# Optimization experiments

Hardware: AMD Instinct MI355X
Metric: run time of the kernel (lower is better)

## Reference

```python
import jax, jax.numpy as jnp
import numpy as np

L = 8        # number of node layers in the DAG
D = 64       # width of every node layer
B = 262144   # batch
N_CONN = L * (L - 1) // 2  # 28 all-to-all forward connections


def setup_inputs() -> dict:
    key = jax.random.key(0)
    kx, kw, kb = jax.random.split(key, 3)
    x = jax.random.normal(kx, (B, D), dtype=jnp.float32)
    # connection weights, torch Linear convention: y = x @ W.T + b, W is [out, in]
    Ws = jax.random.normal(kw, (N_CONN, D, D), dtype=jnp.float32) * (1.0 / np.sqrt(D))
    bs = jax.random.normal(kb, (N_CONN, D), dtype=jnp.float32) * 0.1
    return {"x": x, "Ws": Ws, "bs": bs}


def reference(x, Ws, bs):
    # outputs[0] = input; outputs[1..L-1] start at zero and accumulate messages.
    outs = [x] + [jnp.zeros((x.shape[0], D), dtype=x.dtype) for _ in range(L - 1)]
    # Same iteration order as the torch double loop: source i ascending,
    # target offset i2 ascending; connection c maps layer i -> layer i+i2+1.
    c = 0
    for i in range(L):
        for i2 in range(L - 1 - i):
            j = i + i2 + 1
            outs[j] = outs[j] + jax.nn.relu(outs[i] @ Ws[c].T + bs[c])
            c += 1
    return outs[L - 1]
```

## Files before the change

kernel.cpp:

```cpp
#include <hip/hip_runtime.h>


#define DD 64
#define NCONN 28
#define THREADS 256
#define ROWS_PER_BLOCK 64
#define MAT_ELEMS 4096

typedef __bf16 bf16x8 __attribute__((ext_vector_type(8)));
typedef float f32x4 __attribute__((ext_vector_type(4)));
typedef unsigned short u16x8 __attribute__((ext_vector_type(8)));

__device__ constexpr int OFFS[7] = {0, 7, 13, 18, 22, 25, 27};
__device__ constexpr int CONN[28] = {0, 1,7, 2,8,13, 3,9,14,18, 4,10,15,19,22,
                                     5,11,16,20,23,25, 6,12,17,21,24,26,27};

__device__ __forceinline__ unsigned short f2bfu(float f) {
    return __builtin_bit_cast(unsigned short, (__bf16)f);
}

__device__ __forceinline__ f32x4 vmax4(f32x4 a, f32x4 b) {
#if __has_builtin(__builtin_elementwise_max)
    return __builtin_elementwise_max(a, b);
#else
    f32x4 r;
    r[0] = fmaxf(a[0], b[0]); r[1] = fmaxf(a[1], b[1]);
    r[2] = fmaxf(a[2], b[2]); r[3] = fmaxf(a[3], b[3]);
    return r;
#endif
}

__device__ __forceinline__ void gll16(const unsigned short* g, unsigned short* l) {
    __builtin_amdgcn_global_load_lds(
        (const __attribute__((address_space(1))) unsigned int*)g,
        (__attribute__((address_space(3))) unsigned int*)l, 16, 0, 0);
}

__device__ __forceinline__ void lds_barrier() {
    asm volatile("s_waitcnt lgkmcnt(0)" ::: "memory");
    __builtin_amdgcn_s_barrier();
    asm volatile("" ::: "memory");
}

__global__ void wconv_kernel(const float* __restrict__ w,
                             unsigned short* __restrict__ o) {
    int i = blockIdx.x * blockDim.x + threadIdx.x;
    if (i >= NCONN * 512) return;
    int conn = i >> 9;
    int within = i & 511;
    int r  = within >> 3;
    int k0 = (within & 7) << 3;
    const float* src = w + conn * MAT_ELEMS + r * DD + k0;
    float4 v0 = *reinterpret_cast<const float4*>(src);
    float4 v1 = *reinterpret_cast<const float4*>(src + 4);
    u16x8 d;
    d[0] = f2bfu(v0.x); d[1] = f2bfu(v0.y); d[2] = f2bfu(v0.z); d[3] = f2bfu(v0.w);
    d[4] = f2bfu(v1.x); d[5] = f2bfu(v1.y); d[6] = f2bfu(v1.z); d[7] = f2bfu(v1.w);
    *reinterpret_cast<u16x8*>(o + conn * MAT_ELEMS + r * DD + (k0 ^ ((r & 7) << 3))) = d;
}

template <bool GLL>
__global__ __launch_bounds__(THREADS, 3)
void dag_kernel(const float* __restrict__ x,
                const float* __restrict__ Wf,
                const unsigned short* __restrict__ Wimg,
                const float* __restrict__ bs,
                float* __restrict__ out) {
    __shared__ __align__(16) unsigned short ring[4 * MAT_ELEMS];
    __shared__ __align__(16) unsigned short sB[2 * 2048];
    __shared__ __align__(16) float sBias[NCONN * DD];

    const int tid  = threadIdx.x;
    const int lane = tid & 63;
    const int wv   = tid >> 6;
    const int pair = wv >> 1;
    const int h    = wv & 1;
    const int l15  = lane & 15;
    const int kg   = lane >> 4;

    const long rowbase = (long)blockIdx.x * ROWS_PER_BLOCK + pair * 32;

    for (int idx = tid; idx < NCONN * DD / 4; idx += THREADS)
        reinterpret_cast<float4*>(sBias)[idx] = reinterpret_cast<const float4*>(bs)[idx];

    bf16x8 afrag[7][2][2];
#pragma unroll
    for (int rt = 0; rt < 2; ++rt) {
        const float* xr = x + (rowbase + rt * 16 + l15) * DD;
#pragma unroll
        for (int s = 0; s < 2; ++s) {
            float4 v0 = *reinterpret_cast<const float4*>(xr + s * 32 + kg * 8);
            float4 v1 = *reinterpret_cast<const float4*>(xr + s * 32 + kg * 8 + 4);
            bf16x8 f;
            f[0] = (__bf16)v0.x; f[1] = (__bf16)v0.y; f[2] = (__bf16)v0.z; f[3] = (__bf16)v0.w;
            f[4] = (__bf16)v1.x; f[5] = (__bf16)v1.y; f[6] = (__bf16)v1.z; f[7] = (__bf16)v1.w;
            afrag[0][rt][s] = f;
        }
    }

    auto stage_gll = [&](int p) {
        const unsigned short* src = Wimg + CONN[p] * MAT_ELEMS + wv * 512 + lane * 8;
        unsigned short* dst = ring + (p & 3) * MAT_ELEMS + wv * 512;
#pragma unroll
        for (int hh = 0; hh < 2; ++hh)
            gll16(src + hh * 2048, dst + hh * 2048);
    };
    auto stage_direct = [&](int p) {
        const float* wp = Wf + CONN[p] * MAT_ELEMS;
#pragma unroll
        for (int hh = 0; hh < 2; ++hh) {
            const int e0 = hh * 2048 + tid * 8;
            float4 a0 = *reinterpret_cast<const float4*>(wp + e0);
            float4 a1 = *reinterpret_cast<const float4*>(wp + e0 + 4);
            u16x8 d;
            d[0] = f2bfu(a0.x); d[1] = f2bfu(a0.y); d[2] = f2bfu(a0.z); d[3] = f2bfu(a0.w);
            d[4] = f2bfu(a1.x); d[5] = f2bfu(a1.y); d[6] = f2bfu(a1.z); d[7] = f2bfu(a1.w);
            const int r = e0 >> 6, k0 = e0 & 63;
            *reinterpret_cast<u16x8*>(ring + (p & 3) * MAT_ELEMS +
                                      r * DD + (k0 ^ ((r & 7) << 3))) = d;
        }
    };

    if constexpr (GLL) { stage_gll(0); stage_gll(1); }
    __syncthreads();

    unsigned short* myPB = sB + pair * 2048;
    f32x4 acc[2][2];

#pragma unroll
    for (int j = 1; j <= 7; ++j) {
#pragma unroll
        for (int rt = 0; rt < 2; ++rt)
#pragma unroll
            for (int t = 0; t < 2; ++t) {
                acc[rt][t][0] = 0.f; acc[rt][t][1] = 0.f;
                acc[rt][t][2] = 0.f; acc[rt][t][3] = 0.f;
            }

#pragma unroll
        for (int i = 0; i < j; ++i) {
            const int p = j * (j - 1) / 2 + i;
            const int c = OFFS[i] + (j - i - 1);

            if constexpr (GLL) {
                if ((p & 1) == 0) {
                    if (p > 0) __syncthreads();
                    if (p + 2 < NCONN) { stage_gll(p + 2); stage_gll(p + 3); }
                }
            } else {
                __syncthreads();
                stage_direct(p);
                __syncthreads();
            }

            const unsigned short* wsl = ring + (p & 3) * MAT_ELEMS;
            __builtin_amdgcn_s_setprio(1);
#pragma unroll
            for (int t = 0; t < 2; ++t) {
                const int n  = h * 32 + t * 16 + l15;
                const int xo = (n & 7) << 3;
                u16x8 rw0 = *reinterpret_cast<const u16x8*>(wsl + n * DD + ((kg * 8) ^ xo));
                u16x8 rw1 = *reinterpret_cast<const u16x8*>(wsl + n * DD + ((32 + kg * 8) ^ xo));
                const float bv = sBias[c * DD + n];
                const f32x4 b4 = {bv, bv, bv, bv};
#pragma unroll
                for (int rt = 0; rt < 2; ++rt) {
                    f32x4 C = acc[rt][t];
                    C = __builtin_amdgcn_mfma_f32_16x16x32_bf16(
                            afrag[i][rt][0], __builtin_bit_cast(bf16x8, rw0), C, 0, 0, 0);
                    C = __builtin_amdgcn_mfma_f32_16x16x32_bf16(
                            afrag[i][rt][1], __builtin_bit_cast(bf16x8, rw1), C, 0, 0, 0);
                    acc[rt][t] = vmax4(C + b4, acc[rt][t]);
                }
            }
            __builtin_amdgcn_s_setprio(0);
        }

        if (j < 7) {
#pragma unroll
            for (int rt = 0; rt < 2; ++rt)
#pragma unroll
                for (int t = 0; t < 2; ++t) {
                    const int f = h * 32 + t * 16 + l15;
#pragma unroll
                    for (int q = 0; q < 4; ++q) {
                        const int mr = rt * 16 + kg * 4 + q;
                        myPB[mr * DD + (f ^ ((mr & 7) << 3))] = f2bfu(acc[rt][t][q]);
                    }
                }
            lds_barrier();
#pragma unroll
            for (int rt = 0; rt < 2; ++rt)
#pragma unroll
                for (int s = 0; s < 2; ++s) {
                    u16x8 ra = *reinterpret_cast<const u16x8*>(
                        &myPB[(rt * 16 + l15) * DD + ((s * 32 + kg * 8) ^ ((l15 & 7) << 3))]);
                    afrag[j][rt][s] = __builtin_bit_cast(bf16x8, ra);
                }
            lds_barrier();
        } else {
            float* orow = out + rowbase * DD;
#pragma unroll
            for (int rt = 0; rt < 2; ++rt)
#pragma unroll
                for (int t = 0; t < 2; ++t)
#pragma unroll
                    for (int q = 0; q < 4; ++q)
                        orow[(rt * 16 + kg * 4 + q) * DD + h * 32 + t * 16 + l15] =
                            acc[rt][t][q];
        }
    }
}

extern "C" void kernel_launch(void* const* d_in, const int* in_sizes, int n_in,
                              void* d_out, int out_size, void* d_ws, size_t ws_size,
                              hipStream_t stream) {
    const float* x  = (const float*)d_in[0];
    const float* Ws = (const float*)d_in[1];
    const float* bs = (const float*)d_in[2];
    float* out = (float*)d_out;

    const int nrows = in_sizes[0] / DD;
    const int grid  = nrows / ROWS_PER_BLOCK;

    const size_t wbf_bytes = (size_t)NCONN * MAT_ELEMS * sizeof(unsigned short);
    if (ws_size >= wbf_bytes) {
        unsigned short* wbf = (unsigned short*)d_ws;
        wconv_kernel<<<(NCONN * 512 + 255) / 256, 256, 0, stream>>>(Ws, wbf);
        dag_kernel<true><<<grid, THREADS, 0, stream>>>(x, Ws, wbf, bs, out);
    } else {
        dag_kernel<false><<<grid, THREADS, 0, stream>>>(x, Ws, nullptr, bs, out);
    }
}
```

Baseline: 102.4 us.

## Shrink block to 32 rows with four waves each owning a 16-column slice

Halves rows per block to 32 so all four waves share one 32-row tile, each computing a 16-output-column slice instead of two wave pairs splitting 64 rows. This doubles grid size and halves per-wave accumulators and register pressure, which may raise occupancy, but weight staging from global/L2 is amortized over half as many rows. Bias is now folded into the MFMA accumulator input rather than added afterwards.

Result: slower. 150.8 us (+47.3%).

```diff
diff --git a/kernel.cpp b/kernel.cpp
--- a/kernel.cpp
+++ b/kernel.cpp
@@ -4,7 +4,7 @@
 #define DD 64
 #define NCONN 28
 #define THREADS 256
-#define ROWS_PER_BLOCK 64
+#define ROWS_PER_BLOCK 32
 #define MAT_ELEMS 4096
 
 typedef __bf16 bf16x8 __attribute__((ext_vector_type(8)));
@@ -67,18 +67,16 @@
                 const float* __restrict__ bs,
                 float* __restrict__ out) {
     __shared__ __align__(16) unsigned short ring[4 * MAT_ELEMS];
-    __shared__ __align__(16) unsigned short sB[2 * 2048];
+    __shared__ __align__(16) unsigned short sB[2048];
     __shared__ __align__(16) float sBias[NCONN * DD];
 
     const int tid  = threadIdx.x;
     const int lane = tid & 63;
     const int wv   = tid >> 6;
-    const int pair = wv >> 1;
-    const int h    = wv & 1;
     const int l15  = lane & 15;
     const int kg   = lane >> 4;
 
-    const long rowbase = (long)blockIdx.x * ROWS_PER_BLOCK + pair * 32;
+    const long rowbase = (long)blockIdx.x * ROWS_PER_BLOCK;
 
     for (int idx = tid; idx < NCONN * DD / 4; idx += THREADS)
         reinterpret_cast<float4*>(sBias)[idx] = reinterpret_cast<const float4*>(bs)[idx];
@@ -99,11 +97,11 @@
     }
 
     auto stage_gll = [&](int p) {
-        const unsigned short* src = Wimg + CONN[p] * MAT_ELEMS + wv * 512 + lane * 8;
-        unsigned short* dst = ring + (p & 3) * MAT_ELEMS + wv * 512;
+        const unsigned short* src = Wimg + CONN[p] * MAT_ELEMS + wv * 1024 + lane * 8;
+        unsigned short* dst = ring + (p & 3) * MAT_ELEMS + wv * 1024;
 #pragma unroll
         for (int hh = 0; hh < 2; ++hh)
-            gll16(src + hh * 2048, dst + hh * 2048);
+            gll16(src + hh * 512, dst + hh * 512);
     };
     auto stage_direct = [&](int p) {
         const float* wp = Wf + CONN[p] * MAT_ELEMS;
@@ -124,18 +122,14 @@
     if constexpr (GLL) { stage_gll(0); stage_gll(1); }
     __syncthreads();
 
-    unsigned short* myPB = sB + pair * 2048;
-    f32x4 acc[2][2];
+    f32x4 acc[2];
 
 #pragma unroll
     for (int j = 1; j <= 7; ++j) {
 #pragma unroll
-        for (int rt = 0; rt < 2; ++rt)
-#pragma unroll
-            for (int t = 0; t < 2; ++t) {
-                acc[rt][t][0] = 0.f; acc[rt][t][1] = 0.f;
-                acc[rt][t][2] = 0.f; acc[rt][t][3] = 0.f;
-            }
+        for (int rt = 0; rt < 2; ++rt) {
+            acc[rt][0] = 0.f; acc[rt][1] = 0.f; acc[rt][2] = 0.f; acc[rt][3] = 0.f;
+        }
 
 #pragma unroll
         for (int i = 0; i < j; ++i) {
@@ -154,47 +148,43 @@
             }
 
             const unsigned short* wsl = ring + (p & 3) * MAT_ELEMS;
+            const int n  = wv * 16 + l15;
+            const int xo = (n & 7) << 3;
+            u16x8 rw0 = *reinterpret_cast<const u16x8*>(wsl + n * DD + ((kg * 8) ^ xo));
+            u16x8 rw1 = *reinterpret_cast<const u16x8*>(wsl + n * DD + ((32 + kg * 8) ^ xo));
+            const float bv = sBias[c * DD + n];
+            const f32x4 b4 = {bv, bv, bv, bv};
+
             __builtin_amdgcn_s_setprio(1);
 #pragma unroll
-            for (int t = 0; t < 2; ++t) {
-                const int n  = h * 32 + t * 16 + l15;
-                const int xo = (n & 7) << 3;
-                u16x8 rw0 = *reinterpret_cast<const u16x8*>(wsl + n * DD + ((kg * 8) ^ xo));
-                u16x8 rw1 = *reinterpret_cast<const u16x8*>(wsl + n * DD + ((32 + kg * 8) ^ xo));
-                const float bv = sBias[c * DD + n];
-                const f32x4 b4 = {bv, bv, bv, bv};
-#pragma unroll
-                for (int rt = 0; rt < 2; ++rt) {
-                    f32x4 C = acc[rt][t];
-                    C = __builtin_amdgcn_mfma_f32_16x16x32_bf16(
-                            afrag[i][rt][0], __builtin_bit_cast(bf16x8, rw0), C, 0, 0, 0);
-                    C = __builtin_amdgcn_mfma_f32_16x16x32_bf16(
-                            afrag[i][rt][1], __builtin_bit_cast(bf16x8, rw1), C, 0, 0, 0);
-                    acc[rt][t] = vmax4(C + b4, acc[rt][t]);
+            for (int rt = 0; rt < 2; ++rt) {
+                f32x4 C = acc[rt] + b4;
+                C = __builtin_amdgcn_mfma_f32_16x16x32_bf16(
+                        afrag[i][rt][0], __builtin_bit_cast(bf16x8, rw0), C, 0, 0, 0);
+                C = __builtin_amdgcn_mfma_f32_16x16x32_bf16(
+                        afrag[i][rt][1], __builtin_bit_cast(bf16x8, rw1), C, 0, 0, 0);
+                acc[rt] = vmax4(C, acc[rt]);
+            }
+            __builtin_amdgcn_s_setprio(0);
+        }
+
+        if (j < 7) {
+#pragma unroll
+            for (int rt = 0; rt < 2; ++rt) {
+                const int f = wv * 16 + l15;
+#pragma unroll
+                for (int q = 0; q < 4; ++q) {
+                    const int mr = rt * 16 + kg * 4 + q;
+                    sB[mr * DD + (f ^ ((mr & 7) << 3))] = f2bfu(acc[rt][q]);
                 }
             }
-            __builtin_amdgcn_s_setprio(0);
-        }
-
-        if (j < 7) {
-#pragma unroll
-            for (int rt = 0; rt < 2; ++rt)
-#pragma unroll
-                for (int t = 0; t < 2; ++t) {
-                    const int f = h * 32 + t * 16 + l15;
-#pragma unroll
-                    for (int q = 0; q < 4; ++q) {
-                        const int mr = rt * 16 + kg * 4 + q;
-                        myPB[mr * DD + (f ^ ((mr & 7) << 3))] = f2bfu(acc[rt][t][q]);
-                    }
-                }
             lds_barrier();
 #pragma unroll
             for (int rt = 0; rt < 2; ++rt)
 #pragma unroll
                 for (int s = 0; s < 2; ++s) {
                     u16x8 ra = *reinterpret_cast<const u16x8*>(
-                        &myPB[(rt * 16 + l15) * DD + ((s * 32 + kg * 8) ^ ((l15 & 7) << 3))]);
+                        &sB[(rt * 16 + l15) * DD + ((s * 32 + kg * 8) ^ ((l15 & 7) << 3))]);
                     afrag[j][rt][s] = __builtin_bit_cast(bf16x8, ra);
                 }
             lds_barrier();
@@ -203,11 +193,8 @@
 #pragma unroll
             for (int rt = 0; rt < 2; ++rt)
 #pragma unroll
-                for (int t = 0; t < 2; ++t)
-#pragma unroll
-                    for (int q = 0; q < 4; ++q)
-                        orow[(rt * 16 + kg * 4 + q) * DD + h * 32 + t * 16 + l15] =
-                            acc[rt][t][q];
+                for (int q = 0; q < 4; ++q)
+                    orow[(rt * 16 + kg * 4 + q) * DD + wv * 16 + l15] = acc[rt][q];
         }
     }
 }
```

## Halve rows per block, prefetch bias into registers, fold bias into MFMA accumulator

Applied to the files above, without the earlier changes.

Each block now handles 32 rows instead of 64, so each wave pair computes one 16-row tile rather than two. This cuts the afrag/acc register footprint, and the occupancy hint rises from 3 to 4. The shared-memory bias table is replaced by per-connection bias values loaded into registers alongside the weight prefetch. The bias is now added to the accumulator input before the MFMA instead of after it. The trade-off is that each staged weight matrix is reused across half as many rows, which doubles weight LDS traffic and global weight loads per output row.

After: 130.5 us. 27.5% more time.

```diff
diff --git a/kernel.cpp b/kernel.cpp
--- a/kernel.cpp
+++ b/kernel.cpp
@@ -4,7 +4,7 @@
 #define DD 64
 #define NCONN 28
 #define THREADS 256
-#define ROWS_PER_BLOCK 64
+#define ROWS_PER_BLOCK 32
 #define MAT_ELEMS 4096
 
 typedef __bf16 bf16x8 __attribute__((ext_vector_type(8)));
@@ -60,15 +60,14 @@
 }
 
 template <bool GLL>
-__global__ __launch_bounds__(THREADS, 3)
+__global__ __launch_bounds__(THREADS, 4)
 void dag_kernel(const float* __restrict__ x,
                 const float* __restrict__ Wf,
                 const unsigned short* __restrict__ Wimg,
                 const float* __restrict__ bs,
                 float* __restrict__ out) {
     __shared__ __align__(16) unsigned short ring[4 * MAT_ELEMS];
-    __shared__ __align__(16) unsigned short sB[2 * 2048];
-    __shared__ __align__(16) float sBias[NCONN * DD];
+    __shared__ __align__(16) unsigned short sB[2 * 1024];
 
     const int tid  = threadIdx.x;
     const int lane = tid & 63;
@@ -78,15 +77,11 @@
     const int l15  = lane & 15;
     const int kg   = lane >> 4;
 
-    const long rowbase = (long)blockIdx.x * ROWS_PER_BLOCK + pair * 32;
-
-    for (int idx = tid; idx < NCONN * DD / 4; idx += THREADS)
-        reinterpret_cast<float4*>(sBias)[idx] = reinterpret_cast<const float4*>(bs)[idx];
-
-    bf16x8 afrag[7][2][2];
-#pragma unroll
-    for (int rt = 0; rt < 2; ++rt) {
-        const float* xr = x + (rowbase + rt * 16 + l15) * DD;
+    const long rowbase = (long)blockIdx.x * ROWS_PER_BLOCK + pair * 16;
+
+    bf16x8 afrag[7][2];
+    {
+        const float* xr = x + (rowbase + l15) * DD;
 #pragma unroll
         for (int s = 0; s < 2; ++s) {
             float4 v0 = *reinterpret_cast<const float4*>(xr + s * 32 + kg * 8);
@@ -94,9 +89,16 @@
             bf16x8 f;
             f[0] = (__bf16)v0.x; f[1] = (__bf16)v0.y; f[2] = (__bf16)v0.z; f[3] = (__bf16)v0.w;
             f[4] = (__bf16)v1.x; f[5] = (__bf16)v1.y; f[6] = (__bf16)v1.z; f[7] = (__bf16)v1.w;
-            afrag[0][rt][s] = f;
+            afrag[0][s] = f;
         }
     }
+
+    float breg[2][2][2];
+    auto loadBias = [&](int p) {
+        const float* bp = bs + CONN[p] * DD + h * 32 + l15;
+        float* b = breg[(p >> 1) & 1][p & 1];
+        b[0] = bp[0]; b[1] = bp[16];
+    };
 
     auto stage_gll = [&](int p) {
         const unsigned short* src = Wimg + CONN[p] * MAT_ELEMS + wv * 512 + lane * 8;
@@ -121,39 +123,39 @@
         }
     };
 
+    loadBias(0); loadBias(1);
     if constexpr (GLL) { stage_gll(0); stage_gll(1); }
     __syncthreads();
 
-    unsigned short* myPB = sB + pair * 2048;
-    f32x4 acc[2][2];
+    unsigned short* myPB = sB + pair * 1024;
+    f32x4 acc[2];
 
 #pragma unroll
     for (int j = 1; j <= 7; ++j) {
 #pragma unroll
-        for (int rt = 0; rt < 2; ++rt)
-#pragma unroll
-            for (int t = 0; t < 2; ++t) {
-                acc[rt][t][0] = 0.f; acc[rt][t][1] = 0.f;
-                acc[rt][t][2] = 0.f; acc[rt][t][3] = 0.f;
-            }
+        for (int t = 0; t < 2; ++t) {
+            acc[t][0] = 0.f; acc[t][1] = 0.f; acc[t][2] = 0.f; acc[t][3] = 0.f;
+        }
 
 #pragma unroll
         for (int i = 0; i < j; ++i) {
             const int p = j * (j - 1) / 2 + i;
-            const int c = OFFS[i] + (j - i - 1);
 
             if constexpr (GLL) {
                 if ((p & 1) == 0) {
                     if (p > 0) __syncthreads();
+                    if (p + 2 < NCONN) { loadBias(p + 2); loadBias(p + 3); }
                     if (p + 2 < NCONN) { stage_gll(p + 2); stage_gll(p + 3); }
                 }
             } else {
                 __syncthreads();
                 stage_direct(p);
+                loadBias(p);
                 __syncthreads();
             }
 
             const unsigned short* wsl = ring + (p & 3) * MAT_ELEMS;
+            const float* bv = breg[(p >> 1) & 1][p & 1];
             __builtin_amdgcn_s_setprio(1);
 #pragma unroll
             for (int t = 0; t < 2; ++t) {
@@ -161,53 +163,42 @@
                 const int xo = (n & 7) << 3;
                 u16x8 rw0 = *reinterpret_cast<const u16x8*>(wsl + n * DD + ((kg * 8) ^ xo));
                 u16x8 rw1 = *reinterpret_cast<const u16x8*>(wsl + n * DD + ((32 + kg * 8) ^ xo));
-                const float bv = sBias[c * DD + n];
-                const f32x4 b4 = {bv, bv, bv, bv};
-#pragma unroll
-                for (int rt = 0; rt < 2; ++rt) {
-                    f32x4 C = acc[rt][t];
-                    C = __builtin_amdgcn_mfma_f32_16x16x32_bf16(
-                            afrag[i][rt][0], __builtin_bit_cast(bf16x8, rw0), C, 0, 0, 0);
-                    C = __builtin_amdgcn_mfma_f32_16x16x32_bf16(
-                            afrag[i][rt][1], __builtin_bit_cast(bf16x8, rw1), C, 0, 0, 0);
-                    acc[rt][t] = vmax4(C + b4, acc[rt][t]);
+                const f32x4 b4 = {bv[t], bv[t], bv[t], bv[t]};
+                f32x4 C = acc[t] + b4;
+                C = __builtin_amdgcn_mfma_f32_16x16x32_bf16(
+                        afrag[i][0], __builtin_bit_cast(bf16x8, rw0), C, 0, 0, 0);
+                C = __builtin_amdgcn_mfma_f32_16x16x32_bf16(
+                        afrag[i][1], __builtin_bit_cast(bf16x8, rw1), C, 0, 0, 0);
+                acc[t] = vmax4(C, acc[t]);
+            }
+            __builtin_amdgcn_s_setprio(0);
+        }
+
+        if (j < 7) {
+#pragma unroll
+            for (int t = 0; t < 2; ++t) {
+                const int f = h * 32 + t * 16 + l15;
+#pragma unroll
+                for (int q = 0; q < 4; ++q) {
+                    const int mr = kg * 4 + q;
+                    myPB[mr * DD + (f ^ ((mr & 7) << 3))] = f2bfu(acc[t][q]);
                 }
             }
-            __builtin_amdgcn_s_setprio(0);
-        }
-
-        if (j < 7) {
-#pragma unroll
-            for (int rt = 0; rt < 2; ++rt)
-#pragma unroll
-                for (int t = 0; t < 2; ++t) {
-                    const int f = h * 32 + t * 16 + l15;
-#pragma unroll
-                    for (int q = 0; q < 4; ++q) {
-                        const int mr = rt * 16 + kg * 4 + q;
-                        myPB[mr * DD + (f ^ ((mr & 7) << 3))] = f2bfu(acc[rt][t][q]);
-                    }
-                }
             lds_barrier();
 #pragma unroll
-            for (int rt = 0; rt < 2; ++rt)
-#pragma unroll
-                for (int s = 0; s < 2; ++s) {
-                    u16x8 ra = *reinterpret_cast<const u16x8*>(
-                        &myPB[(rt * 16 + l15) * DD + ((s * 32 + kg * 8) ^ ((l15 & 7) << 3))]);
-                    afrag[j][rt][s] = __builtin_bit_cast(bf16x8, ra);
-                }
+            for (int s = 0; s < 2; ++s) {
+                u16x8 ra = *reinterpret_cast<const u16x8*>(
+                    &myPB[l15 * DD + ((s * 32 + kg * 8) ^ ((l15 & 7) << 3))]);
+                afrag[j][s] = __builtin_bit_cast(bf16x8, ra);
+            }
             lds_barrier();
         } else {
             float* orow = out + rowbase * DD;
 #pragma unroll
-            for (int rt = 0; rt < 2; ++rt)
-#pragma unroll
-                for (int t = 0; t < 2; ++t)
-#pragma unroll
-                    for (int q = 0; q < 4; ++q)
-                        orow[(rt * 16 + kg * 4 + q) * DD + h * 32 + t * 16 + l15] =
-                            acc[rt][t][q];
+            for (int t = 0; t < 2; ++t)
+#pragma unroll
+                for (int q = 0; q < 4; ++q)
+                    orow[(kg * 4 + q) * DD + h * 32 + t * 16 + l15] = acc[t][q];
         }
     }
 }
```

## Split weight staging between LDS ring and direct register prefetch; bias into registers

Applied to the files above, without the earlier changes.

Even-numbered connection weights are still staged through the LDS ring via global_load_lds. Odd-numbered ones are now prefetched from global memory straight into per-wave register buffers (wregA/wregB) two connections ahead. Biases are also loaded directly from global into a small register double-buffer instead of being copied into a shared-memory table. This halves LDS traffic for weights and drops the bias LDS array. In exchange it adds register pressure, which may hurt occupancy, and duplicates global/L2 reads per wave for the odd weights.

After: 213.5 us. +108.5%, slower.

```diff
diff --git a/kernel.cpp b/kernel.cpp
--- a/kernel.cpp
+++ b/kernel.cpp
@@ -68,7 +68,6 @@
                 float* __restrict__ out) {
     __shared__ __align__(16) unsigned short ring[4 * MAT_ELEMS];
     __shared__ __align__(16) unsigned short sB[2 * 2048];
-    __shared__ __align__(16) float sBias[NCONN * DD];
 
     const int tid  = threadIdx.x;
     const int lane = tid & 63;
@@ -80,9 +79,6 @@
 
     const long rowbase = (long)blockIdx.x * ROWS_PER_BLOCK + pair * 32;
 
-    for (int idx = tid; idx < NCONN * DD / 4; idx += THREADS)
-        reinterpret_cast<float4*>(sBias)[idx] = reinterpret_cast<const float4*>(bs)[idx];
-
     bf16x8 afrag[7][2][2];
 #pragma unroll
     for (int rt = 0; rt < 2; ++rt) {
@@ -98,9 +94,30 @@
         }
     }
 
+    float breg[2][2][2];
+    auto loadBias = [&](int p) {
+        const float* bp = bs + CONN[p] * DD + h * 32 + l15;
+        float* b = breg[(p >> 1) & 1][p & 1];
+        b[0] = bp[0]; b[1] = bp[16];
+    };
+
+    u16x8 wregA[4], wregB[4];
+    auto loadWreg = [&](int p, u16x8* dst) {
+        const unsigned short* base = Wimg + CONN[p] * MAT_ELEMS;
+#pragma unroll
+        for (int t = 0; t < 2; ++t) {
+            const int n  = h * 32 + t * 16 + l15;
+            const int xo = (n & 7) << 3;
+#pragma unroll
+            for (int s = 0; s < 2; ++s)
+                dst[t * 2 + s] = *reinterpret_cast<const u16x8*>(
+                    base + n * DD + (((s * 32 + kg * 8)) ^ xo));
+        }
+    };
+
     auto stage_gll = [&](int p) {
         const unsigned short* src = Wimg + CONN[p] * MAT_ELEMS + wv * 512 + lane * 8;
-        unsigned short* dst = ring + (p & 3) * MAT_ELEMS + wv * 512;
+        unsigned short* dst = ring + ((p >> 1) & 3) * MAT_ELEMS + wv * 512;
 #pragma unroll
         for (int hh = 0; hh < 2; ++hh)
             gll16(src + hh * 2048, dst + hh * 2048);
@@ -121,7 +138,8 @@
         }
     };
 
-    if constexpr (GLL) { stage_gll(0); stage_gll(1); }
+    loadBias(0); loadBias(1);
+    if constexpr (GLL) { stage_gll(0); stage_gll(2); loadWreg(1, wregA); }
     __syncthreads();
 
     unsigned short* myPB = sB + pair * 2048;
@@ -140,29 +158,39 @@
 #pragma unroll
         for (int i = 0; i < j; ++i) {
             const int p = j * (j - 1) / 2 + i;
-            const int c = OFFS[i] + (j - i - 1);
 
             if constexpr (GLL) {
                 if ((p & 1) == 0) {
                     if (p > 0) __syncthreads();
-                    if (p + 2 < NCONN) { stage_gll(p + 2); stage_gll(p + 3); }
+                    if (p + 4 <= 26) stage_gll(p + 4);
+                    if (p + 2 < NCONN) { loadBias(p + 2); loadBias(p + 3); }
+                    if (p + 3 < NCONN)
+                        loadWreg(p + 3, (((p >> 1) + 1) & 1) ? wregB : wregA);
                 }
             } else {
                 __syncthreads();
                 stage_direct(p);
+                loadBias(p);
                 __syncthreads();
             }
 
-            const unsigned short* wsl = ring + (p & 3) * MAT_ELEMS;
+            const float* bv = breg[(p >> 1) & 1][p & 1];
             __builtin_amdgcn_s_setprio(1);
 #pragma unroll
             for (int t = 0; t < 2; ++t) {
-                const int n  = h * 32 + t * 16 + l15;
-                const int xo = (n & 7) << 3;
-                u16x8 rw0 = *reinterpret_cast<const u16x8*>(wsl + n * DD + ((kg * 8) ^ xo));
-                u16x8 rw1 = *reinterpret_cast<const u16x8*>(wsl + n * DD + ((32 + kg * 8) ^ xo));
-                const float bv = sBias[c * DD + n];
-                const f32x4 b4 = {bv, bv, bv, bv};
+                u16x8 rw0, rw1;
+                if (!GLL || (p & 1) == 0) {
+                    const unsigned short* wsl =
+                        ring + (GLL ? ((p >> 1) & 3) : (p & 3)) * MAT_ELEMS;
+                    const int n  = h * 32 + t * 16 + l15;
+                    const int xo = (n & 7) << 3;
+                    rw0 = *reinterpret_cast<const u16x8*>(wsl + n * DD + ((kg * 8) ^ xo));
+                    rw1 = *reinterpret_cast<const u16x8*>(wsl + n * DD + ((32 + kg * 8) ^ xo));
+                } else {
+                    const u16x8* wb = ((p >> 1) & 1) ? wregB : wregA;
+                    rw0 = wb[t * 2 + 0]; rw1 = wb[t * 2 + 1];
+                }
+                const f32x4 b4 = {bv[t], bv[t], bv[t], bv[t]};
 #pragma unroll
                 for (int rt = 0; rt < 2; ++rt) {
                     f32x4 C = acc[rt][t];
```
